# Kernel tuning notes

Measured on AMD Instinct MI355X. Metric: run time of the kernel, lower is better.

## Reference

```python
import jax, jax.numpy as jnp
import numpy as np
import math

D = 112          # d_model
H = 28           # n_heads
HD = D // H      # head_dim = 4
L = 2            # num_transformers
NC = 2           # num_classes
GRID_SIZE = 5
SPLINE_ORDER = 3
NB = GRID_SIZE + SPLINE_ORDER  # 8 basis functions
B, S = 16, 512


def make_grid():
    # uniform grid buffer, shape [in_features, grid_size + 2*spline_order + 1] = [112, 12]
    h = 2.0 / GRID_SIZE  # (grid_range[1]-grid_range[0]) / grid_size
    g = jnp.arange(-SPLINE_ORDER, GRID_SIZE + SPLINE_ORDER + 1, dtype=jnp.float32) * h - 1.0
    return jnp.broadcast_to(g, (D, g.shape[0]))


def setup_inputs() -> dict:
    key = jax.random.key(0)
    ks = jax.random.split(key, 20)
    sc = 1.0 / math.sqrt(D)
    inp = {
        'x': jax.random.normal(ks[0], (B, S, D), jnp.float32),
        'attention_mask': jnp.ones((B, S), jnp.int32),
        'grid': make_grid(),
        # per-layer attention params, stacked over L layers
        'qw': jax.random.normal(ks[1], (L, D, D), jnp.float32) * sc,
        'qb': jnp.zeros((L, D), jnp.float32),
        'kw': jax.random.normal(ks[2], (L, D, D), jnp.float32) * sc,
        'kb': jnp.zeros((L, D), jnp.float32),
        'vw': jax.random.normal(ks[3], (L, D, D), jnp.float32) * sc,
        'vb': jnp.zeros((L, D), jnp.float32),
        'ow': jax.random.normal(ks[4], (L, D, D), jnp.float32) * sc,
        'ob': jnp.zeros((L, D), jnp.float32),
        'ln1_g': jnp.ones((L, D), jnp.float32),
        'ln1_b': jnp.zeros((L, D), jnp.float32),
        'ln2_g': jnp.ones((L, D), jnp.float32),
        'ln2_b': jnp.zeros((L, D), jnp.float32),
        # KANLinear params (in=out=D), stacked over L layers
        'base_w': jax.random.normal(ks[5], (L, D, D), jnp.float32) * sc,
        'spline_w': jax.random.normal(ks[6], (L, D, D, NB), jnp.float32) * 0.02,
        'spline_scaler': jax.random.normal(ks[7], (L, D, D), jnp.float32) * sc,
        # classifier
        'cls_w': jax.random.normal(ks[8], (NC, D), jnp.float32) * sc,
        'cls_b': jnp.zeros((NC,), jnp.float32),
    }
    return inp


def layer_norm(x, g, b, eps=1e-5):
    mu = jnp.mean(x, axis=-1, keepdims=True)
    var = jnp.var(x, axis=-1, keepdims=True)
    return (x - mu) * jax.lax.rsqrt(var + eps) * g + b


def b_splines(x, grid):
    # x: [N, in], grid: [in, G]  ->  [N, in, grid_size + spline_order]
    xe = x[:, :, None]
    bases = ((xe >= grid[:, :-1]) & (xe < grid[:, 1:])).astype(x.dtype)
    for k in range(1, SPLINE_ORDER + 1):
        left = (xe - grid[:, :-(k + 1)]) / (grid[:, k:-1] - grid[:, :-(k + 1)]) * bases[:, :, :-1]
        right = (grid[:, k + 1:] - xe) / (grid[:, k + 1:] - grid[:, 1:-k]) * bases[:, :, 1:]
        bases = left + right
    return bases


def kan_linear(x, grid, base_w, spline_w, spline_scaler):
    # x: [N, D] -> [N, D]
    base_out = jax.nn.silu(x) @ base_w.T
    bsp = b_splines(x, grid).reshape(x.shape[0], -1)          # [N, D*NB]
    sw = (spline_w * spline_scaler[:, :, None]).reshape(D, -1)  # [D, D*NB]
    return base_out + bsp @ sw.T


def attention(x, mask, qw, qb, kw, kb, vw, vb, ow, ob):
    b, s, _ = x.shape
    def shape_heads(t):
        return t.reshape(b, s, H, HD).transpose(0, 2, 1, 3)  # [B,H,S,hd]
    q = shape_heads(x @ qw.T + qb) / math.sqrt(HD)
    k = shape_heads(x @ kw.T + kb)
    v = shape_heads(x @ vw.T + vb)
    scores = jnp.einsum('bhqd,bhkd->bhqk', q, k)
    scores = jnp.where(mask[:, None, None, :] == 0, -1e9, scores)
    w = jax.nn.softmax(scores, axis=-1)
    ctx = jnp.einsum('bhqk,bhkd->bhqd', w, v)
    ctx = ctx.transpose(0, 2, 1, 3).reshape(b, s, D)
    return ctx @ ow.T + ob


def reference(x, attention_mask, grid, qw, qb, kw, kb, vw, vb, ow, ob,
              ln1_g, ln1_b, ln2_g, ln2_b, base_w, spline_w, spline_scaler,
              cls_w, cls_b):
    h = x
    for l in range(L):
        a = attention(h, attention_mask, qw[l], qb[l], kw[l], kb[l],
                      vw[l], vb[l], ow[l], ob[l])
        h = layer_norm(h + a, ln1_g[l], ln1_b[l])
        flat = h.reshape(-1, D)
        ff = kan_linear(flat, grid, base_w[l], spline_w[l], spline_scaler[l]).reshape(h.shape)
        h = layer_norm(h + ff, ln2_g[l], ln2_b[l])
    cls = h[:, 0]  # CLS pooling
    return cls @ cls_w.T + cls_b
```

## Files before the change

kernel.cpp:

```cpp
#include <hip/hip_runtime.h>
#include <hip/hip_bf16.h>

#define D 112
#define HEADS 28
#define HDIM 4
#define SEQ 512
#define BATCH 16
#define NTOK (BATCH*SEQ)
#define NBASES 8
#define NKNOT 12
#define KTOT (D*9)
#define KPAD 1024
#define NKT (KPAD/32)
#define TM 16
#define QJT 21
#define PST 20
#define VST 520
#define LOG2E 1.44269504088896f
#define ATTN_BIAS (-23.0831169f)

typedef __attribute__((ext_vector_type(8))) __bf16 bf16x8;
typedef __attribute__((ext_vector_type(4))) float f32x4;

__device__ __forceinline__ unsigned short f2bf(float f) {
    unsigned u = __float_as_uint(f);
    unsigned r = u + 0x7FFFu + ((u >> 16) & 1u);
    return (unsigned short)(r >> 16);
}

__device__ __forceinline__ unsigned cvt_pk_bf16(float lo, float hi) {
    unsigned r;
    asm("v_cvt_pk_bf16_f32 %0, %1, %2" : "=v"(r) : "v"(lo), "v"(hi));
    return r;
}

__global__ void wqkv_prep_kernel(
    const float* __restrict__ qw, const float* __restrict__ kw, const float* __restrict__ vw,
    unsigned short* __restrict__ wq)
{
    int idx = blockIdx.x * 256 + threadIdx.x;
    if (idx >= 2*4*336*32) return;
    int kk = idx & 31;
    int j  = (idx >> 5) % 336;
    int kt = ((idx >> 5) / 336) & 3;
    int l  = idx / (32*336*4);
    int i = kt*32 + kk;
    float val = 0.f;
    if (i < D) {
        int mo = j / D, jj = j % D;
        const float* src = (mo==0) ? qw : (mo==1) ? kw : vw;
        val = src[((size_t)l*D + jj)*D + i];
    }
    wq[idx] = f2bf(val);
}

__global__ void wo_prep_kernel(const float* __restrict__ ow, unsigned short* __restrict__ wo)
{
    int idx = blockIdx.x * 256 + threadIdx.x;
    if (idx >= 2*4*D*32) return;
    int kk = idx & 31;
    int j  = (idx >> 5) % D;
    int kt = ((idx >> 5) / D) & 3;
    int l  = idx / (32*D*4);
    int i = kt*32 + kk;
    float val = (i < D) ? ow[((size_t)l*D + j)*D + i] : 0.f;
    wo[idx] = f2bf(val);
}

__global__ __launch_bounds__(512) void qkv_mfma_kernel(
    const float* __restrict__ hin, const unsigned short* __restrict__ wq,
    const float* __restrict__ qb, const float* __restrict__ kb, const float* __restrict__ vb,
    int l, float* __restrict__ q, float* __restrict__ k, float* __restrict__ v)
{
    __shared__ __align__(16) unsigned short act[TM][136];
    int tid = threadIdx.x;
    int t0 = blockIdx.x * TM;
    for (int e = tid; e < TM*D; e += 512) {
        int t = e / D, i = e % D;
        act[t][i] = f2bf(hin[(size_t)(t0 + t)*D + i]);
    }
    for (int e = tid; e < TM*16; e += 512) act[e/16][D + (e%16)] = 0;
    __syncthreads();

    int w = tid >> 6, lane = tid & 63, m = lane & 15, g4 = lane >> 4;
    f32x4 acc[3];
    #pragma unroll
    for (int qq = 0; qq < 3; ++qq) acc[qq] = (f32x4){0.f,0.f,0.f,0.f};
    const bf16x8* wql = (const bf16x8*)wq + (size_t)l*4*336*4;
    #pragma unroll
    for (int kt = 0; kt < 4; ++kt) {
        bf16x8 a = *(const bf16x8*)&act[m][kt*32 + g4*8];
        #pragma unroll
        for (int qq = 0; qq < 3; ++qq) {
            int jt = w + 8*qq;
            if (jt < QJT) {
                bf16x8 bf = wql[((size_t)kt*336 + jt*16 + m)*4 + g4];
                acc[qq] = __builtin_amdgcn_mfma_f32_16x16x32_bf16(a, bf, acc[qq], 0, 0, 0);
            }
        }
    }
    #pragma unroll
    for (int qq = 0; qq < 3; ++qq) {
        int jt = w + 8*qq;
        if (jt >= QJT) continue;
        int j = jt*16 + m;
        int mo = j / D, jj = j % D;
        const float* bb = (mo==0) ? qb : (mo==1) ? kb : vb;
        float bias = bb[l*D + jj];
        float scl = (mo==0) ? 0.5f*LOG2E : 1.0f;
        float* dst = (mo==0) ? q : (mo==1) ? k : v;
        int h = jj >> 2, hd = jj & 3;
        #pragma unroll
        for (int r = 0; r < 4; ++r) {
            int n = t0 + g4*4 + r;
            int bi = n >> 9, s = n & 511;
            dst[((size_t)(bi*HEADS + h)*SEQ + s)*HDIM + hd] = (acc[qq][r] + bias)*scl;
        }
    }
}

__global__ __launch_bounds__(256) void attn_mfma_kernel(
    const float* __restrict__ q, const float* __restrict__ k, const float* __restrict__ v,
    const int* __restrict__ mask, float* __restrict__ ctx)
{
    __shared__ __align__(16) unsigned short kpack[SEQ][8];
    __shared__ __align__(16) unsigned short qpack[128][8];
    __shared__ __align__(16) unsigned short vT[5][VST];
    __shared__ __align__(16) uint4 zfrag;
    __shared__ __align__(16) unsigned int plds[4][2][16*PST];

    int tid = threadIdx.x;
    int bh = blockIdx.x >> 2, qh = blockIdx.x & 3;
    int b = bh / HEADS, h = bh % HEADS;

    if (tid == 0) zfrag = (uint4){0,0,0,0};
    const float4* kk = (const float4*)k + (size_t)bh*SEQ;
    const float4* vv = (const float4*)v + (size_t)bh*SEQ;
    for (int s = tid; s < SEQ; s += 256) {
        float4 kf = kk[s];
        float mf = mask[b*SEQ + s] ? ATTN_BIAS : -1e9f;
        uint4 pk;
        pk.x = cvt_pk_bf16(kf.x, kf.y);
        pk.y = cvt_pk_bf16(kf.z, kf.w);
        pk.z = cvt_pk_bf16(mf, 0.f);
        pk.w = 0;
        *(uint4*)&kpack[s][0] = pk;
        float4 vf = vv[s];
        vT[0][s] = f2bf(vf.x); vT[1][s] = f2bf(vf.y);
        vT[2][s] = f2bf(vf.z); vT[3][s] = f2bf(vf.w);
        vT[4][s] = 0x3F80;
    }
    if (tid < 128) {
        int s = qh*128 + tid;
        float4 qf = ((const float4*)q)[(size_t)bh*SEQ + s];
        uint4 pk;
        pk.x = cvt_pk_bf16(qf.x, qf.y);
        pk.y = cvt_pk_bf16(qf.z, qf.w);
        pk.z = cvt_pk_bf16(1.0f, 0.f);
        pk.w = 0;
        *(uint4*)&qpack[tid][0] = pk;
    }
    __syncthreads();

    int w = tid >> 6, lane = tid & 63, ln = lane & 15, g4 = lane >> 4;
    const bf16x8* zf = (const bf16x8*)&zfrag;
    unsigned int* pw0 = &plds[w][0][0];
    unsigned int* pw1 = &plds[w][1][0];

    for (int qt = 0; qt < 2; ++qt) {
        int q0 = w*32 + qt*16;
        bf16x8 qfrag = (g4 == 0) ? *(const bf16x8*)&qpack[q0 + ln][0] : *zf;
        f32x4 oacc = {0.f,0.f,0.f,0.f};
        #pragma unroll 2
        for (int kb = 0; kb < SEQ; kb += 64) {
            int kcA = kb, kcB = kb + 32;
            bf16x8 kaA0 = (g4 == 0) ? *(const bf16x8*)&kpack[kcA + ln][0]      : *zf;
            bf16x8 kaA1 = (g4 == 0) ? *(const bf16x8*)&kpack[kcA + 16 + ln][0] : *zf;
            bf16x8 kaB0 = (g4 == 0) ? *(const bf16x8*)&kpack[kcB + ln][0]      : *zf;
            bf16x8 kaB1 = (g4 == 0) ? *(const bf16x8*)&kpack[kcB + 16 + ln][0] : *zf;
            f32x4 sA0 = __builtin_amdgcn_mfma_f32_16x16x32_bf16(kaA0, qfrag, (f32x4){0.f,0.f,0.f,0.f}, 0, 0, 0);
            f32x4 sA1 = __builtin_amdgcn_mfma_f32_16x16x32_bf16(kaA1, qfrag, (f32x4){0.f,0.f,0.f,0.f}, 0, 0, 0);
            f32x4 sB0 = __builtin_amdgcn_mfma_f32_16x16x32_bf16(kaB0, qfrag, (f32x4){0.f,0.f,0.f,0.f}, 0, 0, 0);
            f32x4 sB1 = __builtin_amdgcn_mfma_f32_16x16x32_bf16(kaB1, qfrag, (f32x4){0.f,0.f,0.f,0.f}, 0, 0, 0);
            float a00 = __builtin_exp2f(sA0[0]), a01 = __builtin_exp2f(sA0[1]);
            float a02 = __builtin_exp2f(sA0[2]), a03 = __builtin_exp2f(sA0[3]);
            float a10 = __builtin_exp2f(sA1[0]), a11 = __builtin_exp2f(sA1[1]);
            float a12 = __builtin_exp2f(sA1[2]), a13 = __builtin_exp2f(sA1[3]);
            float b00 = __builtin_exp2f(sB0[0]), b01 = __builtin_exp2f(sB0[1]);
            float b02 = __builtin_exp2f(sB0[2]), b03 = __builtin_exp2f(sB0[3]);
            float b10 = __builtin_exp2f(sB1[0]), b11 = __builtin_exp2f(sB1[1]);
            float b12 = __builtin_exp2f(sB1[2]), b13 = __builtin_exp2f(sB1[3]);
            uint2 wA0 = {cvt_pk_bf16(a00, a01), cvt_pk_bf16(a02, a03)};
            uint2 wA1 = {cvt_pk_bf16(a10, a11), cvt_pk_bf16(a12, a13)};
            uint2 wB0 = {cvt_pk_bf16(b00, b01), cvt_pk_bf16(b02, b03)};
            uint2 wB1 = {cvt_pk_bf16(b10, b11), cvt_pk_bf16(b12, b13)};
            *(uint2*)&pw0[ln*PST + g4*2]     = wA0;
            *(uint2*)&pw0[ln*PST + 8 + g4*2] = wA1;
            *(uint2*)&pw1[ln*PST + g4*2]     = wB0;
            *(uint2*)&pw1[ln*PST + 8 + g4*2] = wB1;
            bf16x8 paA = *(const bf16x8*)&pw0[ln*PST + g4*4];
            bf16x8 vbA = (ln < 5) ? *(const bf16x8*)&vT[ln][kcA + g4*8] : *zf;
            oacc = __builtin_amdgcn_mfma_f32_16x16x32_bf16(paA, vbA, oacc, 0, 0, 0);
            bf16x8 paB = *(const bf16x8*)&pw1[ln*PST + g4*4];
            bf16x8 vbB = (ln < 5) ? *(const bf16x8*)&vT[ln][kcB + g4*8] : *zf;
            oacc = __builtin_amdgcn_mfma_f32_16x16x32_bf16(paB, vbB, oacc, 0, 0, 0);
        }
        int src = g4*16 + 4;
        float s0 = __shfl(oacc[0], src, 64);
        float s1 = __shfl(oacc[1], src, 64);
        float s2 = __shfl(oacc[2], src, 64);
        float s3 = __shfl(oacc[3], src, 64);
        float i0 = __builtin_amdgcn_rcpf(s0);
        float i1 = __builtin_amdgcn_rcpf(s1);
        float i2 = __builtin_amdgcn_rcpf(s2);
        float i3 = __builtin_amdgcn_rcpf(s3);
        if (ln < 4) {
            size_t base = (size_t)(b*SEQ + qh*128 + q0 + g4*4);
            ctx[(base + 0)*D + h*4 + ln] = oacc[0] * i0;
            ctx[(base + 1)*D + h*4 + ln] = oacc[1] * i1;
            ctx[(base + 2)*D + h*4 + ln] = oacc[2] * i2;
            ctx[(base + 3)*D + h*4 + ln] = oacc[3] * i3;
        }
    }
}

__global__ void wb_prep_kernel(
    const float* __restrict__ base_w, const float* __restrict__ spline_w,
    const float* __restrict__ scaler, unsigned short* __restrict__ wb)
{
    int idx = blockIdx.x * 256 + threadIdx.x;
    if (idx >= 2 * NKT * D * 32) return;
    int kk = idx & 31;
    int j  = (idx >> 5) % D;
    int kt = ((idx >> 5) / D) % NKT;
    int l  = idx / (32 * D * NKT);
    int k = kt * 32 + kk;
    float val = 0.f;
    if (k < KTOT) {
        int i = k / 9, b = k % 9;
        size_t ji = ((size_t)l * D + j) * D + i;
        val = (b == 8) ? base_w[ji] : spline_w[ji * NBASES + b] * scaler[ji];
    }
    wb[idx] = f2bf(val);
}

__global__ __launch_bounds__(512) void oproj_kan_ln_kernel(
    const float* __restrict__ ctx, const float* __restrict__ hin,
    const unsigned short* __restrict__ wo, const float* __restrict__ ob,
    const float* __restrict__ g1, const float* __restrict__ b1,
    const float* __restrict__ grid, const unsigned short* __restrict__ wb,
    const float* __restrict__ g2, const float* __restrict__ b2,
    int l, int gstride, float* __restrict__ hout)
{
    __shared__ __align__(16) unsigned short abuf[TM*1032];
    __shared__ float so[TM][D];
    int tid = threadIdx.x;
    int t0 = blockIdx.x * TM;
    int w = tid >> 6, lane = tid & 63, m = lane & 15, g4 = lane >> 4;
    int jw = w*16 + m;

    float resv[4], obv = 0.f;
    if (w < 7) {
        obv = ob[l*D + jw];
        #pragma unroll
        for (int r = 0; r < 4; ++r)
            resv[r] = hin[(size_t)(t0 + g4*4 + r)*D + jw];
    }

    for (int e = tid; e < TM*136; e += 512) {
        int t = e / 136, i = e % 136;
        abuf[e] = (i < D) ? f2bf(ctx[(size_t)(t0 + t)*D + i]) : 0;
    }
    __syncthreads();

    if (w < 7) {
        f32x4 acc = {0.f,0.f,0.f,0.f};
        const bf16x8* wol = (const bf16x8*)wo + (size_t)l*4*D*4;
        #pragma unroll
        for (int kt = 0; kt < 4; ++kt) {
            bf16x8 a = *(const bf16x8*)&abuf[m*136 + kt*32 + g4*8];
            bf16x8 b0 = wol[((size_t)kt*D + jw)*4 + g4];
            acc = __builtin_amdgcn_mfma_f32_16x16x32_bf16(a, b0, acc, 0, 0, 0);
        }
        #pragma unroll
        for (int r = 0; r < 4; ++r)
            so[g4*4 + r][jw] = acc[r] + obv + resv[r];
    }
    __syncthreads();

    for (int tt = 0; tt < 2; ++tt) {
        int t = w*2 + tt;
        float x0 = so[t][lane];
        float x1 = (lane + 64 < D) ? so[t][lane + 64] : 0.f;
        float s1 = x0 + x1, s2 = x0*x0 + x1*x1;
        #pragma unroll
        for (int off = 32; off; off >>= 1) { s1 += __shfl_xor(s1, off, 64); s2 += __shfl_xor(s2, off, 64); }
        float mu = s1 * (1.f/112.f);
        float var = s2 * (1.f/112.f) - mu*mu;
        float rs = rsqrtf(var + 1e-5f);
        so[t][lane] = (x0 - mu)*rs*g1[l*D + lane] + b1[l*D + lane];
        if (lane + 64 < D)
            so[t][lane+64] = (x1 - mu)*rs*g1[l*D + lane+64] + b1[l*D + lane+64];
    }
    __syncthreads();

    for (int e = tid; e < TM * D; e += 512) {
        int tk = e / D, i = e % D;
        float xv = so[tk][i];
        float si = xv * __builtin_amdgcn_rcpf(1.f + __expf(-xv));
        const float* grp = grid + i * gstride;
        float gz = grp[0];
        float hh = grp[1] - gz;
        float u = (xv - gz) / hh;
        float fidx = floorf(u);
        int idx = (int)fidx;
        float t = u - fidx;
        float t2 = t*t, t3 = t2*t;
        const float s6 = 1.f/6.f;
        float p0 = t3 * s6;
        float p1 = (-3.f*t3 + 3.f*t2 + 3.f*t + 1.f) * s6;
        float p2 = (3.f*t3 - 6.f*t2 + 4.f) * s6;
        float om = 1.f - t;
        float p3 = om*om*om * s6;
        unsigned short* arow = &abuf[tk*1032 + i*9];
        #pragma unroll
        for (int b = 0; b < 8; ++b) arow[b] = 0;
        if (u >= 0.f && idx <= 10) {
            if (idx <= 7) arow[idx]   = f2bf(p0);
            if (idx >= 1 && idx <= 8) arow[idx-1] = f2bf(p1);
            if (idx >= 2 && idx <= 9) arow[idx-2] = f2bf(p2);
            if (idx >= 3)             arow[idx-3] = f2bf(p3);
        }
        arow[8] = f2bf(si);
    }
    for (int e = tid; e < TM * 24; e += 512)
        abuf[(e/24)*1032 + KTOT + (e%24)] = 0;
    __syncthreads();

    if (w < 7) {
        f32x4 acc = {0.f,0.f,0.f,0.f};
        const bf16x8* wbl = (const bf16x8*)wb + (size_t)l * NKT * D * 4;
        #pragma unroll 4
        for (int kt = 0; kt < NKT; ++kt) {
            bf16x8 a = *(const bf16x8*)&abuf[m*1032 + kt*32 + g4*8];
            bf16x8 b0 = wbl[((size_t)kt*D + jw)*4 + g4];
            acc = __builtin_amdgcn_mfma_f32_16x16x32_bf16(a, b0, acc, 0, 0, 0);
        }
        #pragma unroll
        for (int r = 0; r < 4; ++r) {
            int t = g4*4 + r;
            so[t][jw] = acc[r] + so[t][jw];
        }
    }
    __syncthreads();

    for (int tt = 0; tt < 2; ++tt) {
        int t = w*2 + tt;
        float x0 = so[t][lane];
        float x1 = (lane + 64 < D) ? so[t][lane + 64] : 0.f;
        float s1 = x0 + x1, s2 = x0*x0 + x1*x1;
        #pragma unroll
        for (int off = 32; off; off >>= 1) { s1 += __shfl_xor(s1, off, 64); s2 += __shfl_xor(s2, off, 64); }
        float mu = s1 * (1.f/112.f);
        float var = s2 * (1.f/112.f) - mu*mu;
        float rs = rsqrtf(var + 1e-5f);
        for (int ii = lane; ii < D; ii += 64)
            hout[(size_t)(t0 + t)*D + ii] = (so[t][ii] - mu)*rs*g2[l*D + ii] + b2[l*D + ii];
    }
}

__global__ __launch_bounds__(64) void cls_kernel(
    const float* __restrict__ h, const float* __restrict__ cw, const float* __restrict__ cb,
    float* __restrict__ out)
{
    int tid = threadIdx.x;
    if (tid < BATCH*2) {
        int b = tid >> 1, c = tid & 1;
        const float* hr = h + (size_t)b*SEQ*D;
        const float* wr = cw + c*D;
        float a = 0.f;
        for (int i = 0; i < D; ++i) a += hr[i]*wr[i];
        out[b*2 + c] = a + cb[c];
    }
}

__global__ void sentinel_kernel(float* __restrict__ out, int nel)
{
    int i = threadIdx.x;
    if (i < nel) out[i] = 1e30f;
}

extern "C" void kernel_launch(void* const* d_in, const int* in_sizes, int n_in,
                              void* d_out, int out_size, void* d_ws, size_t ws_size,
                              hipStream_t stream)
{
    const float* x      = (const float*)d_in[0];
    const int*   mask   = (const int*)  d_in[1];
    const float* grid   = (const float*)d_in[2];
    const float* qw     = (const float*)d_in[3];
    const float* qb     = (const float*)d_in[4];
    const float* kw     = (const float*)d_in[5];
    const float* kb     = (const float*)d_in[6];
    const float* vw     = (const float*)d_in[7];
    const float* vb     = (const float*)d_in[8];
    const float* ow     = (const float*)d_in[9];
    const float* ob     = (const float*)d_in[10];
    const float* ln1g   = (const float*)d_in[11];
    const float* ln1b   = (const float*)d_in[12];
    const float* ln2g   = (const float*)d_in[13];
    const float* ln2b   = (const float*)d_in[14];
    const float* base_w = (const float*)d_in[15];
    const float* spline_w = (const float*)d_in[16];
    const float* scaler = (const float*)d_in[17];
    const float* cls_w  = (const float*)d_in[18];
    const float* cls_b  = (const float*)d_in[19];

    size_t SZ   = (size_t)NTOK * D;
    size_t WBN  = (size_t)2 * NKT * D * 32;
    size_t WQN  = (size_t)2 * 4 * 336 * 32;
    size_t WON  = (size_t)2 * 4 * D * 32;
    size_t need = 6*SZ*sizeof(float) + (WBN + WQN + WON)*sizeof(unsigned short) + 256;
    if (ws_size < need) {
        sentinel_kernel<<<1, 64, 0, stream>>>((float*)d_out, out_size);
        return;
    }
    float* ws = (float*)d_ws;
    float* q   = ws;
    float* k   = q + SZ;
    float* v   = k + SZ;
    float* ctx = v + SZ;
    float* hA  = ctx + SZ;
    float* hB  = hA + SZ;
    unsigned short* wbuf  = (unsigned short*)(hB + SZ);
    unsigned short* wqkv  = wbuf + WBN;
    unsigned short* wobuf = wqkv + WQN;

    int gstride = (in_sizes[2] == NKNOT) ? 0 : NKNOT;

    wb_prep_kernel<<<(int)((WBN + 255)/256), 256, 0, stream>>>(base_w, spline_w, scaler, wbuf);
    wqkv_prep_kernel<<<(int)((WQN + 255)/256), 256, 0, stream>>>(qw, kw, vw, wqkv);
    wo_prep_kernel<<<(int)((WON + 255)/256), 256, 0, stream>>>(ow, wobuf);

    const float* hin = x;
    float* houts[2] = {hA, hB};
    for (int l = 0; l < 2; ++l) {
        qkv_mfma_kernel<<<NTOK/TM, 512, 0, stream>>>(hin, wqkv, qb, kb, vb, l, q, k, v);
        attn_mfma_kernel<<<BATCH*HEADS*4, 256, 0, stream>>>(q, k, v, mask, ctx);
        oproj_kan_ln_kernel<<<NTOK/TM, 512, 0, stream>>>(ctx, hin, wobuf, ob, ln1g, ln1b,
                                                         grid, wbuf, ln2g, ln2b, l, gstride, houts[l]);
        hin = houts[l];
    }
    cls_kernel<<<1, 64, 0, stream>>>(hB, cls_w, cls_b, (float*)d_out);
}
```

Baseline: 154.0 us.

## Switch attention to 32x32x16 MFMA with register shuffles instead of LDS staging

Rewrites the attention kernel to use 32x32x16 bf16 MFMAs, so each wave covers 32 queries in a single pass rather than two 16-query tiles. Score probabilities are turned into the P*V operand with cross-half wave shuffles instead of being written to and reread from LDS. The Q tile is loaded straight into registers, which drops its LDS staging and the zero fragment. Each lane now writes ctx as one float4. The gain is meant to come from less LDS traffic and fewer instructions, at the cost of tricky fragment-layout assumptions that must match the MFMA operand format exactly.

```diff
diff --git a/kernel.cpp b/kernel.cpp
--- a/kernel.cpp
+++ b/kernel.cpp
@@ -14,13 +14,14 @@
 #define NKT (KPAD/32)
 #define TM 16
 #define QJT 21
-#define PST 20
+#define KST 12
 #define VST 520
 #define LOG2E 1.44269504088896f
 #define ATTN_BIAS (-23.0831169f)
 
 typedef __attribute__((ext_vector_type(8))) __bf16 bf16x8;
 typedef __attribute__((ext_vector_type(4))) float f32x4;
+typedef __attribute__((ext_vector_type(16))) float f32x16;
 
 __device__ __forceinline__ unsigned short f2bf(float f) {
     unsigned u = __float_as_uint(f);
@@ -123,104 +124,88 @@
     const float* __restrict__ q, const float* __restrict__ k, const float* __restrict__ v,
     const int* __restrict__ mask, float* __restrict__ ctx)
 {
-    __shared__ __align__(16) unsigned short kpack[SEQ][8];
-    __shared__ __align__(16) unsigned short qpack[128][8];
+    __shared__ __align__(16) unsigned short kpack[SEQ][KST];
     __shared__ __align__(16) unsigned short vT[5][VST];
-    __shared__ __align__(16) uint4 zfrag;
-    __shared__ __align__(16) unsigned int plds[4][2][16*PST];
-
     int tid = threadIdx.x;
     int bh = blockIdx.x >> 2, qh = blockIdx.x & 3;
-    int b = bh / HEADS, h = bh % HEADS;
-
-    if (tid == 0) zfrag = (uint4){0,0,0,0};
+    int b = bh / HEADS, hd = bh % HEADS;
+
     const float4* kk = (const float4*)k + (size_t)bh*SEQ;
     const float4* vv = (const float4*)v + (size_t)bh*SEQ;
     for (int s = tid; s < SEQ; s += 256) {
         float4 kf = kk[s];
         float mf = mask[b*SEQ + s] ? ATTN_BIAS : -1e9f;
-        uint4 pk;
-        pk.x = cvt_pk_bf16(kf.x, kf.y);
-        pk.y = cvt_pk_bf16(kf.z, kf.w);
-        pk.z = cvt_pk_bf16(mf, 0.f);
-        pk.w = 0;
-        *(uint4*)&kpack[s][0] = pk;
+        *(uint2*)&kpack[s][0] = (uint2){cvt_pk_bf16(kf.x, kf.y), cvt_pk_bf16(kf.z, kf.w)};
+        *(uint2*)&kpack[s][4] = (uint2){cvt_pk_bf16(mf, 0.f), 0u};
         float4 vf = vv[s];
         vT[0][s] = f2bf(vf.x); vT[1][s] = f2bf(vf.y);
         vT[2][s] = f2bf(vf.z); vT[3][s] = f2bf(vf.w);
         vT[4][s] = 0x3F80;
     }
-    if (tid < 128) {
-        int s = qh*128 + tid;
-        float4 qf = ((const float4*)q)[(size_t)bh*SEQ + s];
-        uint4 pk;
-        pk.x = cvt_pk_bf16(qf.x, qf.y);
-        pk.y = cvt_pk_bf16(qf.z, qf.w);
-        pk.z = cvt_pk_bf16(1.0f, 0.f);
-        pk.w = 0;
-        *(uint4*)&qpack[tid][0] = pk;
-    }
-    __syncthreads();
-
-    int w = tid >> 6, lane = tid & 63, ln = lane & 15, g4 = lane >> 4;
-    const bf16x8* zf = (const bf16x8*)&zfrag;
-    unsigned int* pw0 = &plds[w][0][0];
-    unsigned int* pw1 = &plds[w][1][0];
-
-    for (int qt = 0; qt < 2; ++qt) {
-        int q0 = w*32 + qt*16;
-        bf16x8 qfrag = (g4 == 0) ? *(const bf16x8*)&qpack[q0 + ln][0] : *zf;
-        f32x4 oacc = {0.f,0.f,0.f,0.f};
-        #pragma unroll 2
-        for (int kb = 0; kb < SEQ; kb += 64) {
-            int kcA = kb, kcB = kb + 32;
-            bf16x8 kaA0 = (g4 == 0) ? *(const bf16x8*)&kpack[kcA + ln][0]      : *zf;
-            bf16x8 kaA1 = (g4 == 0) ? *(const bf16x8*)&kpack[kcA + 16 + ln][0] : *zf;
-            bf16x8 kaB0 = (g4 == 0) ? *(const bf16x8*)&kpack[kcB + ln][0]      : *zf;
-            bf16x8 kaB1 = (g4 == 0) ? *(const bf16x8*)&kpack[kcB + 16 + ln][0] : *zf;
-            f32x4 sA0 = __builtin_amdgcn_mfma_f32_16x16x32_bf16(kaA0, qfrag, (f32x4){0.f,0.f,0.f,0.f}, 0, 0, 0);
-            f32x4 sA1 = __builtin_amdgcn_mfma_f32_16x16x32_bf16(kaA1, qfrag, (f32x4){0.f,0.f,0.f,0.f}, 0, 0, 0);
-            f32x4 sB0 = __builtin_amdgcn_mfma_f32_16x16x32_bf16(kaB0, qfrag, (f32x4){0.f,0.f,0.f,0.f}, 0, 0, 0);
-            f32x4 sB1 = __builtin_amdgcn_mfma_f32_16x16x32_bf16(kaB1, qfrag, (f32x4){0.f,0.f,0.f,0.f}, 0, 0, 0);
-            float a00 = __builtin_exp2f(sA0[0]), a01 = __builtin_exp2f(sA0[1]);
-            float a02 = __builtin_exp2f(sA0[2]), a03 = __builtin_exp2f(sA0[3]);
-            float a10 = __builtin_exp2f(sA1[0]), a11 = __builtin_exp2f(sA1[1]);
-            float a12 = __builtin_exp2f(sA1[2]), a13 = __builtin_exp2f(sA1[3]);
-            float b00 = __builtin_exp2f(sB0[0]), b01 = __builtin_exp2f(sB0[1]);
-            float b02 = __builtin_exp2f(sB0[2]), b03 = __builtin_exp2f(sB0[3]);
-            float b10 = __builtin_exp2f(sB1[0]), b11 = __builtin_exp2f(sB1[1]);
-            float b12 = __builtin_exp2f(sB1[2]), b13 = __builtin_exp2f(sB1[3]);
-            uint2 wA0 = {cvt_pk_bf16(a00, a01), cvt_pk_bf16(a02, a03)};
-            uint2 wA1 = {cvt_pk_bf16(a10, a11), cvt_pk_bf16(a12, a13)};
-            uint2 wB0 = {cvt_pk_bf16(b00, b01), cvt_pk_bf16(b02, b03)};
-            uint2 wB1 = {cvt_pk_bf16(b10, b11), cvt_pk_bf16(b12, b13)};
-            *(uint2*)&pw0[ln*PST + g4*2]     = wA0;
-            *(uint2*)&pw0[ln*PST + 8 + g4*2] = wA1;
-            *(uint2*)&pw1[ln*PST + g4*2]     = wB0;
-            *(uint2*)&pw1[ln*PST + 8 + g4*2] = wB1;
-            bf16x8 paA = *(const bf16x8*)&pw0[ln*PST + g4*4];
-            bf16x8 vbA = (ln < 5) ? *(const bf16x8*)&vT[ln][kcA + g4*8] : *zf;
-            oacc = __builtin_amdgcn_mfma_f32_16x16x32_bf16(paA, vbA, oacc, 0, 0, 0);
-            bf16x8 paB = *(const bf16x8*)&pw1[ln*PST + g4*4];
-            bf16x8 vbB = (ln < 5) ? *(const bf16x8*)&vT[ln][kcB + g4*8] : *zf;
-            oacc = __builtin_amdgcn_mfma_f32_16x16x32_bf16(paB, vbB, oacc, 0, 0, 0);
-        }
-        int src = g4*16 + 4;
-        float s0 = __shfl(oacc[0], src, 64);
-        float s1 = __shfl(oacc[1], src, 64);
-        float s2 = __shfl(oacc[2], src, 64);
-        float s3 = __shfl(oacc[3], src, 64);
-        float i0 = __builtin_amdgcn_rcpf(s0);
-        float i1 = __builtin_amdgcn_rcpf(s1);
-        float i2 = __builtin_amdgcn_rcpf(s2);
-        float i3 = __builtin_amdgcn_rcpf(s3);
-        if (ln < 4) {
-            size_t base = (size_t)(b*SEQ + qh*128 + q0 + g4*4);
-            ctx[(base + 0)*D + h*4 + ln] = oacc[0] * i0;
-            ctx[(base + 1)*D + h*4 + ln] = oacc[1] * i1;
-            ctx[(base + 2)*D + h*4 + ln] = oacc[2] * i2;
-            ctx[(base + 3)*D + h*4 + ln] = oacc[3] * i3;
-        }
+    __syncthreads();
+
+    int w = tid >> 6, lane = tid & 63;
+    int m = lane & 31;
+    int hf = lane >> 5;
+    int q0 = qh*128 + w*32;
+
+    bf16x8 qfrag;
+    {
+        uint4 uq = {0,0,0,0};
+        if (hf == 0) {
+            float4 qf = ((const float4*)q)[(size_t)bh*SEQ + q0 + m];
+            uq = (uint4){cvt_pk_bf16(qf.x, qf.y), cvt_pk_bf16(qf.z, qf.w), 0x3F80u, 0u};
+        }
+        qfrag = *(bf16x8*)&uq;
+    }
+
+    f32x16 oacc = {};
+    #pragma unroll 2
+    for (int kb = 0; kb < SEQ; kb += 32) {
+        bf16x8 kfrag;
+        {
+            uint4 u = {0,0,0,0};
+            if (hf == 0) {
+                uint2 lo = *(const uint2*)&kpack[kb + m][0];
+                uint2 hi = *(const uint2*)&kpack[kb + m][4];
+                u = (uint4){lo.x, lo.y, hi.x, hi.y};
+            }
+            kfrag = *(bf16x8*)&u;
+        }
+        f32x16 sc = {};
+        sc = __builtin_amdgcn_mfma_f32_32x32x16_bf16(kfrag, qfrag, sc, 0, 0, 0);
+        float p0  = __builtin_exp2f(sc[0]),  p1  = __builtin_exp2f(sc[1]);
+        float p2  = __builtin_exp2f(sc[2]),  p3  = __builtin_exp2f(sc[3]);
+        float p4  = __builtin_exp2f(sc[4]),  p5  = __builtin_exp2f(sc[5]);
+        float p6  = __builtin_exp2f(sc[6]),  p7  = __builtin_exp2f(sc[7]);
+        float p8  = __builtin_exp2f(sc[8]),  p9  = __builtin_exp2f(sc[9]);
+        float p10 = __builtin_exp2f(sc[10]), p11 = __builtin_exp2f(sc[11]);
+        float p12 = __builtin_exp2f(sc[12]), p13 = __builtin_exp2f(sc[13]);
+        float p14 = __builtin_exp2f(sc[14]), p15 = __builtin_exp2f(sc[15]);
+        unsigned c0 = cvt_pk_bf16(p0,  p1),  c1 = cvt_pk_bf16(p2,  p3);
+        unsigned c2 = cvt_pk_bf16(p4,  p5),  c3 = cvt_pk_bf16(p6,  p7);
+        unsigned c4 = cvt_pk_bf16(p8,  p9),  c5 = cvt_pk_bf16(p10, p11);
+        unsigned c6 = cvt_pk_bf16(p12, p13), c7 = cvt_pk_bf16(p14, p15);
+        unsigned x0 = __shfl_xor(c0, 32, 64), x1 = __shfl_xor(c1, 32, 64);
+        unsigned x2 = __shfl_xor(c2, 32, 64), x3 = __shfl_xor(c3, 32, 64);
+        unsigned x4 = __shfl_xor(c4, 32, 64), x5 = __shfl_xor(c5, 32, 64);
+        unsigned x6 = __shfl_xor(c6, 32, 64), x7 = __shfl_xor(c7, 32, 64);
+        uint4 uf1 = { hf ? x2 : c0, hf ? x3 : c1, hf ? c2 : x0, hf ? c3 : x1 };
+        uint4 uf2 = { hf ? x6 : c4, hf ? x7 : c5, hf ? c6 : x4, hf ? c7 : x5 };
+        bf16x8 pf1 = *(bf16x8*)&uf1;
+        bf16x8 pf2 = *(bf16x8*)&uf2;
+        uint4 z = {0,0,0,0};
+        bf16x8 va1 = (m < 5) ? *(const bf16x8*)&vT[m][kb + hf*8]      : *(bf16x8*)&z;
+        bf16x8 va2 = (m < 5) ? *(const bf16x8*)&vT[m][kb + 16 + hf*8] : *(bf16x8*)&z;
+        oacc = __builtin_amdgcn_mfma_f32_32x32x16_bf16(va1, pf1, oacc, 0, 0, 0);
+        oacc = __builtin_amdgcn_mfma_f32_32x32x16_bf16(va2, pf2, oacc, 0, 0, 0);
+    }
+    float dn = __shfl_xor(oacc[0], 32, 64);
+    float inv = __builtin_amdgcn_rcpf(dn);
+    if (hf == 0) {
+        int qi = q0 + m;
+        float4 o = {oacc[0]*inv, oacc[1]*inv, oacc[2]*inv, oacc[3]*inv};
+        ((float4*)ctx)[(size_t)(b*SEQ + qi)*HEADS + hd] = o;
     }
 }
 
```

After: 148.9 us. -3.3%, faster.
